# Performance work log

Hardware: AMD Instinct MI355X
Metric: run time of the kernel (lower is better)

## Reference

```python
import jax, jax.numpy as jnp
import numpy as np

IN_DIM = 1024
OUT_DIM = 1024
NUM_EXPERTS = 8
TOP_K = 2
B = 8192


def setup_inputs() -> dict:
    key = jax.random.key(0)
    ks = jax.random.split(key, 8)
    s_in = 1.0 / np.sqrt(IN_DIM)
    s_out = 1.0 / np.sqrt(OUT_DIM)
    return {
        "x": jax.random.normal(ks[0], (B, IN_DIM), dtype=jnp.float32),
        # router Linear(in_dim, num_experts)
        "rw": jax.random.uniform(ks[1], (IN_DIM, NUM_EXPERTS), jnp.float32, -s_in, s_in),
        "rb": jax.random.uniform(ks[2], (NUM_EXPERTS,), jnp.float32, -s_in, s_in),
        # expert MLPs stacked along expert axis
        "w1": jax.random.uniform(ks[3], (NUM_EXPERTS, IN_DIM, OUT_DIM), jnp.float32, -s_in, s_in),
        "b1": jax.random.uniform(ks[4], (NUM_EXPERTS, OUT_DIM), jnp.float32, -s_in, s_in),
        "w2": jax.random.uniform(ks[5], (NUM_EXPERTS, OUT_DIM, OUT_DIM), jnp.float32, -s_out, s_out),
        "b2": jax.random.uniform(ks[6], (NUM_EXPERTS, OUT_DIM), jnp.float32, -s_out, s_out),
    }


def reference(x, rw, rb, w1, b1, w2, b2):
    # ---- TopkRouter ----
    logits = x @ rw + rb                                  # [B, E]
    topk_vals, topk_idx = jax.lax.top_k(logits, TOP_K)    # [B, K]
    neg_inf = jnp.full_like(logits, -jnp.inf)
    rows = jnp.arange(logits.shape[0])[:, None]
    sparse_logits = neg_inf.at[rows, topk_idx].set(topk_vals)
    gating = jax.nn.softmax(sparse_logits, axis=-1)       # zeros outside top-k

    # ---- experts: dense compute, gating weights are exactly 0 for
    # non-selected experts so the weighted combine matches the masked
    # dispatch of the original module. ----
    h = jax.nn.relu(jnp.einsum('bi,eio->beo', x, w1) + b1[None])   # [B, E, out]
    y = jnp.einsum('beh,eho->beo', h, w2) + b2[None]               # [B, E, out]
    fused = jnp.einsum('beo,be->bo', y, gating)                    # [B, out]
    return fused, gating
```

## Files before the change

kernel.cpp:

```cpp
#include <hip/hip_runtime.h>
#include <hip/hip_bf16.h>
#include <cstdint>
#include <cstddef>

#define IN_DIM 1024
#define OUT_DIM 1024
#define NE 8
#define NTOK 8192
#define MT_TILES 20
#define RBLK 512

typedef __bf16 bf16x8 __attribute__((ext_vector_type(8)));
typedef float f32x4 __attribute__((ext_vector_type(4)));
typedef unsigned short ushort8v __attribute__((ext_vector_type(8)));

__device__ __forceinline__ unsigned short f2bf(float f) {
    unsigned u = __float_as_uint(f);
    unsigned r = 0x7fffu + ((u >> 16) & 1u);
    return (unsigned short)((u + r) >> 16);
}

__device__ __forceinline__ void bf2x(unsigned u, float& lo, float& hi) {
    lo = __uint_as_float(u << 16);
    hi = __uint_as_float(u & 0xffff0000u);
}

__device__ __forceinline__ void async16(void* lds, const void* g) {
    __builtin_amdgcn_global_load_lds(
        (const __attribute__((address_space(1))) unsigned int*)g,
        (__attribute__((address_space(3))) unsigned int*)lds,
        16, 0, 0);
}

__device__ __forceinline__ void convert_tile(
    const float* __restrict__ src, unsigned short* __restrict__ dst,
    int kt, int nt, int t, float* tile ) {
    int r = t >> 2, cq = (t & 3) * 16;
#pragma unroll
    for (int q = 0; q < 4; ++q) {
        float4 v = *(const float4*)(src + (size_t)(kt + r) * 1024 + nt + cq + q * 4);
        tile[r * 69 + cq + q * 4 + 0] = v.x;
        tile[r * 69 + cq + q * 4 + 1] = v.y;
        tile[r * 69 + cq + q * 4 + 2] = v.z;
        tile[r * 69 + cq + q * 4 + 3] = v.w;
    }
    __syncthreads();
    int n2 = t >> 3, k8 = (t & 7) * 8;
#pragma unroll
    for (int q = 0; q < 2; ++q) {
        int n = n2 + q * 32;
        ushort8v o;
#pragma unroll
        for (int i = 0; i < 8; ++i) o[i] = f2bf(tile[(k8 + i) * 69 + n]);
        *(ushort8v*)(dst + (size_t)(nt + n) * 1024 + kt + k8) = o;
    }
}

__global__ __launch_bounds__(256) void prep_kernel(
    const float* __restrict__ w1, unsigned short* __restrict__ w1T,
    const float* __restrict__ x, const float* __restrict__ rw,
    const float* __restrict__ rb,
    unsigned short* __restrict__ xb,
    float* __restrict__ gating, int* __restrict__ enc,
    float2* __restrict__ gw, int* __restrict__ cnt) {
    __shared__ float lds_f[NE * IN_DIM];
    int b = blockIdx.x;
    int t = threadIdx.x;
    if (b < RBLK) {
        float* srw = lds_f;
        if (b == 0 && t < NE) cnt[t] = 0;
#pragma unroll
        for (int i = 0; i < 4; ++i) {
            int k = t + i * 256;
            float4 a = *(const float4*)(rw + (size_t)k * NE);
            float4 bq = *(const float4*)(rw + (size_t)k * NE + 4);
            srw[0 * IN_DIM + k] = a.x;  srw[1 * IN_DIM + k] = a.y;
            srw[2 * IN_DIM + k] = a.z;  srw[3 * IN_DIM + k] = a.w;
            srw[4 * IN_DIM + k] = bq.x; srw[5 * IN_DIM + k] = bq.y;
            srw[6 * IN_DIM + k] = bq.z; srw[7 * IN_DIM + k] = bq.w;
        }
        __syncthreads();
        int wave = t >> 6, lane = t & 63;
        for (int tt = 0; tt < 4; ++tt) {
            int tok = b * 16 + wave * 4 + tt;
            const float* xrow = x + (size_t)tok * IN_DIM;
            unsigned short* xbrow = xb + (size_t)tok * IN_DIM;
            float acc[NE] = {0, 0, 0, 0, 0, 0, 0, 0};
#pragma unroll
            for (int i = 0; i < 4; ++i) {
                int k = i * 256 + lane * 4;
                float4 xv = *(const float4*)(xrow + k);
                ushort4 o;
                o.x = f2bf(xv.x); o.y = f2bf(xv.y); o.z = f2bf(xv.z); o.w = f2bf(xv.w);
                *(ushort4*)(xbrow + k) = o;
#pragma unroll
                for (int e = 0; e < NE; ++e) {
                    float4 wv = *(const float4*)(srw + e * IN_DIM + k);
                    acc[e] = fmaf(xv.x, wv.x, fmaf(xv.y, wv.y, fmaf(xv.z, wv.z, fmaf(xv.w, wv.w, acc[e]))));
                }
            }
#pragma unroll
            for (int e = 0; e < NE; ++e) {
#pragma unroll
                for (int off = 32; off > 0; off >>= 1) acc[e] += __shfl_xor(acc[e], off);
                acc[e] += rb[e];
            }
            int e0 = 0; float v0 = acc[0];
#pragma unroll
            for (int e = 1; e < NE; ++e) if (acc[e] > v0) { v0 = acc[e]; e0 = e; }
            int e1 = -1; float v1 = -3.4e38f;
#pragma unroll
            for (int e = 0; e < NE; ++e) if (e != e0 && acc[e] > v1) { v1 = acc[e]; e1 = e; }
            float tg = __expf(v1 - v0);
            float inv = 1.0f / (1.0f + tg);
            float g0 = inv, g1 = tg * inv;
            if (lane < NE) gating[(size_t)tok * NE + lane] = (lane == e0) ? g0 : ((lane == e1) ? g1 : 0.0f);
            if (lane == 0) {
                enc[tok] = e0 | (e1 << 8);
                gw[tok] = make_float2(g0, g1);
            }
        }
    } else {
        int cb = b - RBLK;
        int z = cb >> 8;
        int kt = ((cb >> 4) & 15) * 64, nt = (cb & 15) * 64;
        convert_tile(w1 + (size_t)z * IN_DIM * OUT_DIM,
                     w1T + (size_t)z * IN_DIM * OUT_DIM, kt, nt, t, lds_f);
    }
}

__global__ __launch_bounds__(256) void bucket_kernel(
    const int* __restrict__ enc,
    int* __restrict__ bidx, int* __restrict__ slots, int* __restrict__ cnt,
    const float* __restrict__ w2, unsigned short* __restrict__ w2T) {
    int b = blockIdx.x;
    int t = threadIdx.x;
    if (b < NTOK / 256) {
        int tok = b * 256 + t;
        int lane = t & 63;
        int v = enc[tok];
        int e0 = v & 0xff, e1 = (v >> 8) & 0xff;
        unsigned long long below = (1ull << lane) - 1ull;
        int p0 = 0, p1 = 0;
#pragma unroll
        for (int e = 0; e < NE; ++e) {
            unsigned long long m0 = __ballot(e0 == e);
            unsigned long long m1 = __ballot(e1 == e);
            int c0 = __popcll(m0), c1 = __popcll(m1);
            int base = 0;
            if (lane == 0 && (c0 + c1)) base = atomicAdd(&cnt[e], c0 + c1);
            base = __shfl(base, 0);
            if (e0 == e) p0 = base + __popcll(m0 & below);
            if (e1 == e) p1 = base + c0 + __popcll(m1 & below);
        }
        bidx[e0 * NTOK + p0] = tok;
        bidx[e1 * NTOK + p1] = tok;
        slots[2 * tok + 0] = (e0 << 13) | p0;
        slots[2 * tok + 1] = (e1 << 13) | p1;
    } else {
        __shared__ float tile[64 * 69];
        int cb = b - NTOK / 256;
        int z = cb >> 8;
        int kt = ((cb >> 4) & 15) * 64, nt = (cb & 15) * 64;
        convert_tile(w2 + (size_t)z * OUT_DIM * OUT_DIM,
                     w2T + (size_t)z * OUT_DIM * OUT_DIM, kt, nt, t, tile);
    }
}

__device__ __forceinline__ int prefix_cnt(const int* __restrict__ cnt, int e) {
    int s = 0;
    for (int i = 0; i < NE; ++i) s += (i < e) ? cnt[i] : 0;
    return s;
}

__device__ __forceinline__ void kstep(const unsigned short* Ab,
                                      const unsigned short* Bb,
                                      f32x4 (&acc)[4][4], int wm, int wn,
                                      int lhalf, int slot) {
    bf16x8 av[4], bv[4];
#pragma unroll
    for (int i = 0; i < 4; ++i)
        av[i] = *(const bf16x8*)(Ab + (wm * 32 + i * 8 + lhalf) * 64 + slot);
#pragma unroll
    for (int j = 0; j < 4; ++j)
        bv[j] = *(const bf16x8*)(Bb + (wn * 32 + j * 8 + lhalf) * 64 + slot);
#pragma unroll
    for (int i = 0; i < 4; ++i)
#pragma unroll
        for (int j = 0; j < 4; ++j)
            acc[i][j] = __builtin_amdgcn_mfma_f32_16x16x32_bf16(av[i], bv[j], acc[i][j], 0, 0, 0);
}


__global__ __launch_bounds__(256) void gemm1_kernel(
    const unsigned short* __restrict__ xb, const unsigned short* __restrict__ w1T,
    const float* __restrict__ b1, const int* __restrict__ bidx,
    const int* __restrict__ cnt,
    unsigned short* __restrict__ H) {
    int b = blockIdx.x;
    int e = b & 7;
    int t2 = b >> 3;
    int nt = t2 & 7;
    int mt = t2 >> 3;
    int n_e = cnt[e];
    if (mt * 128 >= n_e) return;
    __shared__ __attribute__((aligned(16))) unsigned short As[3][64 * 64];
    __shared__ __attribute__((aligned(16))) unsigned short Bs[3][64 * 64];
    int t = threadIdx.x, wave = t >> 6, lane = t & 63;
    const int* be = bidx + e * NTOK;
    const unsigned short* agp[2]; const unsigned short* bgp[2];
    int ldsoff[2];
#pragma unroll
    for (int is = 0; is < 2; ++is) {
        int c = is * 256 + t;
        int line = c >> 3;
        int chunkg = (c & 7) ^ (line & 7);
        int sub = chunkg >> 2;
        int growl = 2 * line + sub;
        int growlB = (line >> 5) * 64 + (line & 7) * 8 + sub * 4 + ((line >> 3) & 3);
        int gcol = (chunkg & 3) * 8;
        int gra = mt * 128 + growl;
        int grac = gra < n_e ? gra : n_e - 1;
        agp[is] = xb + (size_t)be[grac] * IN_DIM + gcol;
        bgp[is] = w1T + ((size_t)e * OUT_DIM + nt * 128 + growlB) * IN_DIM + gcol;
        ldsoff[is] = (is * 256 + wave * 64) * 8;
    }
    int wm = wave & 1, wn = wave >> 1;
    int quad = lane >> 4, l15 = lane & 15;
    int lhalf = l15 >> 1;
    int slot = (((l15 & 1) * 4 + quad) ^ lhalf) * 8;
    f32x4 zero4 = {0.f, 0.f, 0.f, 0.f};
    f32x4 acc[4][4];
#pragma unroll
    for (int i = 0; i < 4; ++i)
#pragma unroll
        for (int j = 0; j < 4; ++j) acc[i][j] = zero4;

#pragma unroll
    for (int pt = 0; pt < 2; ++pt)
#pragma unroll
        for (int is = 0; is < 2; ++is) {
            async16(&As[pt][ldsoff[is]], agp[is] + pt * 32);
            async16(&Bs[pt][ldsoff[is]], bgp[is] + pt * 32);
        }
    int cb = 0, sb = 2;
    for (int it = 0; it < 31; ++it) {
        asm volatile("s_waitcnt vmcnt(4)\n\ts_barrier" ::: "memory");
        if (it < 30) {
            int ktn = (it + 2) * 32;
#pragma unroll
            for (int is = 0; is < 2; ++is) {
                async16(&As[sb][ldsoff[is]], agp[is] + ktn);
                async16(&Bs[sb][ldsoff[is]], bgp[is] + ktn);
            }
        }
        kstep(As[cb], Bs[cb], acc, wm, wn, lhalf, slot);
        cb = (cb == 2) ? 0 : cb + 1;
        sb = (sb == 2) ? 0 : sb + 1;
    }
    asm volatile("s_waitcnt vmcnt(0)\n\ts_barrier" ::: "memory");
    kstep(As[cb], Bs[cb], acc, wm, wn, lhalf, slot);

    int hbase = prefix_cnt(cnt, e);
    const float* b1e = b1 + (size_t)e * OUT_DIM;
    int n0 = nt * 128 + wn * 64 + l15 * 4;
    float4 bias = *(const float4*)(b1e + n0);
#pragma unroll
    for (int i = 0; i < 4; ++i) {
        int m0 = mt * 128 + wm * 64 + i * 16 + quad * 4;
#pragma unroll
        for (int r = 0; r < 4; ++r) {
            int gm = m0 + r;
            if (gm < n_e) {
                float h0 = acc[i][0][r] + bias.x; h0 = h0 > 0.f ? h0 : 0.f;
                float h1 = acc[i][1][r] + bias.y; h1 = h1 > 0.f ? h1 : 0.f;
                float h2 = acc[i][2][r] + bias.z; h2 = h2 > 0.f ? h2 : 0.f;
                float h3 = acc[i][3][r] + bias.w; h3 = h3 > 0.f ? h3 : 0.f;
                ushort4 o;
                o.x = f2bf(h0); o.y = f2bf(h1); o.z = f2bf(h2); o.w = f2bf(h3);
                *(ushort4*)(H + (size_t)(hbase + gm) * OUT_DIM + n0) = o;
            }
        }
    }
}

__global__ __launch_bounds__(256) void gemm2_kernel(
    const unsigned short* __restrict__ H, const unsigned short* __restrict__ w2T,
    const int* __restrict__ cnt,
    unsigned short* __restrict__ Y) {
    int b = blockIdx.x;
    int e = b & 7;
    int t2 = b >> 3;
    int nt = t2 & 7;
    int mt = t2 >> 3;
    int n_e = cnt[e];
    if (mt * 128 >= n_e) return;
    __shared__ __attribute__((aligned(16))) unsigned short As[3][64 * 64];
    __shared__ __attribute__((aligned(16))) unsigned short Bs[3][64 * 64];
    int t = threadIdx.x, wave = t >> 6, lane = t & 63;
    int hbase = prefix_cnt(cnt, e);
    const unsigned short* agp[2]; const unsigned short* bgp[2];
    int ldsoff[2];
#pragma unroll
    for (int is = 0; is < 2; ++is) {
        int c = is * 256 + t;
        int line = c >> 3;
        int chunkg = (c & 7) ^ (line & 7);
        int sub = chunkg >> 2;
        int growl = 2 * line + sub;
        int growlB = (line >> 5) * 64 + (line & 7) * 8 + sub * 4 + ((line >> 3) & 3);
        int gcol = (chunkg & 3) * 8;
        int gra = mt * 128 + growl;
        int grac = gra < n_e ? gra : n_e - 1;
        agp[is] = H + (size_t)(hbase + grac) * OUT_DIM + gcol;
        bgp[is] = w2T + ((size_t)e * OUT_DIM + nt * 128 + growlB) * OUT_DIM + gcol;
        ldsoff[is] = (is * 256 + wave * 64) * 8;
    }
    int wm = wave & 1, wn = wave >> 1;
    int quad = lane >> 4, l15 = lane & 15;
    int lhalf = l15 >> 1;
    int slot = (((l15 & 1) * 4 + quad) ^ lhalf) * 8;
    f32x4 zero4 = {0.f, 0.f, 0.f, 0.f};
    f32x4 acc[4][4];
#pragma unroll
    for (int i = 0; i < 4; ++i)
#pragma unroll
        for (int j = 0; j < 4; ++j) acc[i][j] = zero4;

#pragma unroll
    for (int pt = 0; pt < 2; ++pt)
#pragma unroll
        for (int is = 0; is < 2; ++is) {
            async16(&As[pt][ldsoff[is]], agp[is] + pt * 32);
            async16(&Bs[pt][ldsoff[is]], bgp[is] + pt * 32);
        }
    int cb = 0, sb = 2;
    for (int it = 0; it < 31; ++it) {
        asm volatile("s_waitcnt vmcnt(4)\n\ts_barrier" ::: "memory");
        if (it < 30) {
            int ktn = (it + 2) * 32;
#pragma unroll
            for (int is = 0; is < 2; ++is) {
                async16(&As[sb][ldsoff[is]], agp[is] + ktn);
                async16(&Bs[sb][ldsoff[is]], bgp[is] + ktn);
            }
        }
        kstep(As[cb], Bs[cb], acc, wm, wn, lhalf, slot);
        cb = (cb == 2) ? 0 : cb + 1;
        sb = (sb == 2) ? 0 : sb + 1;
    }
    asm volatile("s_waitcnt vmcnt(0)\n\ts_barrier" ::: "memory");
    kstep(As[cb], Bs[cb], acc, wm, wn, lhalf, slot);

    int n0 = nt * 128 + wn * 64 + l15 * 4;
#pragma unroll
    for (int i = 0; i < 4; ++i) {
        int m0 = mt * 128 + wm * 64 + i * 16 + quad * 4;
#pragma unroll
        for (int r = 0; r < 4; ++r) {
            int gm = m0 + r;
            if (gm < n_e) {
                ushort4 o;
                o.x = f2bf(acc[i][0][r]); o.y = f2bf(acc[i][1][r]);
                o.z = f2bf(acc[i][2][r]); o.w = f2bf(acc[i][3][r]);
                *(ushort4*)(Y + (size_t)(hbase + gm) * OUT_DIM + n0) = o;
            }
        }
    }
}

__global__ __launch_bounds__(256) void combine_kernel(
    const unsigned short* __restrict__ Y, const float* __restrict__ b2,
    const float2* __restrict__ gw, const int* __restrict__ slots,
    const int* __restrict__ cnt, float* __restrict__ out) {
    int t = threadIdx.x, wave = t >> 6, lane = t & 63;
    int tok = blockIdx.x * 4 + wave;
    int pre[NE];
    {
        int s = 0;
#pragma unroll
        for (int i = 0; i < NE; ++i) { pre[i] = s; s += cnt[i]; }
    }
    int s0 = slots[2 * tok], s1 = slots[2 * tok + 1];
    int e0 = s0 >> 13, e1 = s1 >> 13;
    int r0 = pre[e0] + (s0 & 8191);
    int r1 = pre[e1] + (s1 & 8191);
    float2 g = gw[tok];
    const unsigned short* y0 = Y + (size_t)r0 * OUT_DIM;
    const unsigned short* y1 = Y + (size_t)r1 * OUT_DIM;
    const float* c0 = b2 + (size_t)e0 * OUT_DIM;
    const float* c1 = b2 + (size_t)e1 * OUT_DIM;
    float* orow = out + (size_t)tok * OUT_DIM;
#pragma unroll
    for (int i = 0; i < 2; ++i) {
        int c = i * 512 + lane * 8;
        uint4 ua = *(const uint4*)(y0 + c);
        uint4 ub = *(const uint4*)(y1 + c);
        float a[8], b[8];
        bf2x(ua.x, a[0], a[1]); bf2x(ua.y, a[2], a[3]);
        bf2x(ua.z, a[4], a[5]); bf2x(ua.w, a[6], a[7]);
        bf2x(ub.x, b[0], b[1]); bf2x(ub.y, b[2], b[3]);
        bf2x(ub.z, b[4], b[5]); bf2x(ub.w, b[6], b[7]);
        float4 p0 = *(const float4*)(c0 + c);
        float4 p1 = *(const float4*)(c0 + c + 4);
        float4 q0 = *(const float4*)(c1 + c);
        float4 q1 = *(const float4*)(c1 + c + 4);
        float o[8];
        o[0] = g.x * (a[0] + p0.x) + g.y * (b[0] + q0.x);
        o[1] = g.x * (a[1] + p0.y) + g.y * (b[1] + q0.y);
        o[2] = g.x * (a[2] + p0.z) + g.y * (b[2] + q0.z);
        o[3] = g.x * (a[3] + p0.w) + g.y * (b[3] + q0.w);
        o[4] = g.x * (a[4] + p1.x) + g.y * (b[4] + q1.x);
        o[5] = g.x * (a[5] + p1.y) + g.y * (b[5] + q1.y);
        o[6] = g.x * (a[6] + p1.z) + g.y * (b[6] + q1.z);
        o[7] = g.x * (a[7] + p1.w) + g.y * (b[7] + q1.w);
        *(float4*)(orow + c) = make_float4(o[0], o[1], o[2], o[3]);
        *(float4*)(orow + c + 4) = make_float4(o[4], o[5], o[6], o[7]);
    }
}

extern "C" void kernel_launch(void* const* d_in, const int* in_sizes, int n_in,
                              void* d_out, int out_size, void* d_ws, size_t ws_size,
                              hipStream_t stream) {
    const float* x  = (const float*)d_in[0];
    const float* rw = (const float*)d_in[1];
    const float* rb = (const float*)d_in[2];
    const float* w1 = (const float*)d_in[3];
    const float* b1 = (const float*)d_in[4];
    const float* w2 = (const float*)d_in[5];
    const float* b2 = (const float*)d_in[6];
    float* out = (float*)d_out;
    float* gating = out + (size_t)NTOK * OUT_DIM;

    char* ws = (char*)d_ws;
    unsigned short* xb  = (unsigned short*)(ws + 0);
    unsigned short* Y   = (unsigned short*)(ws + 0);
    unsigned short* w1T = (unsigned short*)(ws + 16777216);
    unsigned short* w2T = (unsigned short*)(ws + 33554432);
    unsigned short* H   = (unsigned short*)(ws + 50331648);
    int*   bidx  = (int*)(ws + 83886080);
    int*   slots = (int*)(ws + 84148224);
    int*   cnt   = (int*)(ws + 84213760);
    int*    enc  = (int*)(ws + 84213888);
    float2* gw   = (float2*)(ws + 84246656);

    prep_kernel<<<RBLK + 8 * 16 * 16, 256, 0, stream>>>(
        w1, w1T, x, rw, rb, xb, gating, enc, gw, cnt);
    bucket_kernel<<<NTOK / 256 + 8 * 16 * 16, 256, 0, stream>>>(
        enc, bidx, slots, cnt, w2, w2T);
    gemm1_kernel<<<8 * 8 * MT_TILES, 256, 0, stream>>>(xb, w1T, b1, bidx, cnt, H);
    gemm2_kernel<<<8 * 8 * MT_TILES, 256, 0, stream>>>(H, w2T, cnt, Y);
    combine_kernel<<<NTOK / 4, 256, 0, stream>>>(Y, b2, gw, slots, cnt, out);
    (void)in_sizes; (void)n_in; (void)out_size; (void)ws_size;
}
```

Before: 279.0 us.

## Fuse token bucketing and w2 conversion into the router prep kernel

The separate bucket kernel is removed. Each router block now assigns its 16 tokens to expert buckets with a wave-level ballot and atomics right after routing, and the w2 transpose/convert tiles run as extra blocks of the same prep launch. The counter reset moves to a memset before the launch. This saves a kernel launch and the enc round-trip through global memory, at the cost of more atomics (one set per 16 tokens instead of per 64) and a different bucket ordering.

```diff
diff --git a/kernel.cpp b/kernel.cpp
--- a/kernel.cpp
+++ b/kernel.cpp
@@ -57,18 +57,20 @@
 }
 
 __global__ __launch_bounds__(256) void prep_kernel(
-    const float* __restrict__ w1, unsigned short* __restrict__ w1T,
+    const float* __restrict__ w1, const float* __restrict__ w2,
+    unsigned short* __restrict__ w1T, unsigned short* __restrict__ w2T,
     const float* __restrict__ x, const float* __restrict__ rw,
     const float* __restrict__ rb,
     unsigned short* __restrict__ xb,
-    float* __restrict__ gating, int* __restrict__ enc,
-    float2* __restrict__ gw, int* __restrict__ cnt) {
+    float* __restrict__ gating,
+    float2* __restrict__ gw, int* __restrict__ cnt,
+    int* __restrict__ bidx, int* __restrict__ slots) {
     __shared__ float lds_f[NE * IN_DIM];
+    __shared__ int ebuf[32];
     int b = blockIdx.x;
     int t = threadIdx.x;
     if (b < RBLK) {
         float* srw = lds_f;
-        if (b == 0 && t < NE) cnt[t] = 0;
 #pragma unroll
         for (int i = 0; i < 4; ++i) {
             int k = t + i * 256;
@@ -82,7 +84,8 @@
         __syncthreads();
         int wave = t >> 6, lane = t & 63;
         for (int tt = 0; tt < 4; ++tt) {
-            int tok = b * 16 + wave * 4 + tt;
+            int idx = wave * 4 + tt;
+            int tok = b * 16 + idx;
             const float* xrow = x + (size_t)tok * IN_DIM;
             unsigned short* xbrow = xb + (size_t)tok * IN_DIM;
             float acc[NE] = {0, 0, 0, 0, 0, 0, 0, 0};
@@ -116,54 +119,45 @@
             float g0 = inv, g1 = tg * inv;
             if (lane < NE) gating[(size_t)tok * NE + lane] = (lane == e0) ? g0 : ((lane == e1) ? g1 : 0.0f);
             if (lane == 0) {
-                enc[tok] = e0 | (e1 << 8);
+                ebuf[2 * idx + 0] = e0;
+                ebuf[2 * idx + 1] = e1;
                 gw[tok] = make_float2(g0, g1);
             }
         }
-    } else {
+        __syncthreads();
+        if (t < 64) {
+            bool active = t < 32;
+            int myE = active ? ebuf[t] : 0xff;
+            unsigned long long below = (1ull << t) - 1ull;
+            int pos = 0;
+#pragma unroll
+            for (int e = 0; e < NE; ++e) {
+                unsigned long long m = __ballot(active && myE == e);
+                int c = __popcll(m);
+                int base = 0;
+                if (t == 0 && c) base = atomicAdd(&cnt[e], c);
+                base = __shfl(base, 0);
+                if (active && myE == e) pos = base + __popcll(m & below);
+            }
+            if (active) {
+                int tok = b * 16 + (t >> 1);
+                int which = t & 1;
+                bidx[myE * NTOK + pos] = tok;
+                slots[2 * tok + which] = (myE << 13) | pos;
+            }
+        }
+    } else if (b < RBLK + 2048) {
         int cb = b - RBLK;
         int z = cb >> 8;
         int kt = ((cb >> 4) & 15) * 64, nt = (cb & 15) * 64;
         convert_tile(w1 + (size_t)z * IN_DIM * OUT_DIM,
                      w1T + (size_t)z * IN_DIM * OUT_DIM, kt, nt, t, lds_f);
-    }
-}
-
-__global__ __launch_bounds__(256) void bucket_kernel(
-    const int* __restrict__ enc,
-    int* __restrict__ bidx, int* __restrict__ slots, int* __restrict__ cnt,
-    const float* __restrict__ w2, unsigned short* __restrict__ w2T) {
-    int b = blockIdx.x;
-    int t = threadIdx.x;
-    if (b < NTOK / 256) {
-        int tok = b * 256 + t;
-        int lane = t & 63;
-        int v = enc[tok];
-        int e0 = v & 0xff, e1 = (v >> 8) & 0xff;
-        unsigned long long below = (1ull << lane) - 1ull;
-        int p0 = 0, p1 = 0;
-#pragma unroll
-        for (int e = 0; e < NE; ++e) {
-            unsigned long long m0 = __ballot(e0 == e);
-            unsigned long long m1 = __ballot(e1 == e);
-            int c0 = __popcll(m0), c1 = __popcll(m1);
-            int base = 0;
-            if (lane == 0 && (c0 + c1)) base = atomicAdd(&cnt[e], c0 + c1);
-            base = __shfl(base, 0);
-            if (e0 == e) p0 = base + __popcll(m0 & below);
-            if (e1 == e) p1 = base + c0 + __popcll(m1 & below);
-        }
-        bidx[e0 * NTOK + p0] = tok;
-        bidx[e1 * NTOK + p1] = tok;
-        slots[2 * tok + 0] = (e0 << 13) | p0;
-        slots[2 * tok + 1] = (e1 << 13) | p1;
     } else {
-        __shared__ float tile[64 * 69];
-        int cb = b - NTOK / 256;
+        int cb = b - RBLK - 2048;
         int z = cb >> 8;
         int kt = ((cb >> 4) & 15) * 64, nt = (cb & 15) * 64;
         convert_tile(w2 + (size_t)z * OUT_DIM * OUT_DIM,
-                     w2T + (size_t)z * OUT_DIM * OUT_DIM, kt, nt, t, tile);
+                     w2T + (size_t)z * OUT_DIM * OUT_DIM, kt, nt, t, lds_f);
     }
 }
 
@@ -441,13 +435,11 @@
     int*   bidx  = (int*)(ws + 83886080);
     int*   slots = (int*)(ws + 84148224);
     int*   cnt   = (int*)(ws + 84213760);
-    int*    enc  = (int*)(ws + 84213888);
     float2* gw   = (float2*)(ws + 84246656);
 
-    prep_kernel<<<RBLK + 8 * 16 * 16, 256, 0, stream>>>(
-        w1, w1T, x, rw, rb, xb, gating, enc, gw, cnt);
-    bucket_kernel<<<NTOK / 256 + 8 * 16 * 16, 256, 0, stream>>>(
-        enc, bidx, slots, cnt, w2, w2T);
+    hipMemsetAsync(cnt, 0, NE * sizeof(int), stream);
+    prep_kernel<<<RBLK + 4096, 256, 0, stream>>>(
+        w1, w2, w1T, w2T, x, rw, rb, xb, gating, gw, cnt, bidx, slots);
     gemm1_kernel<<<8 * 8 * MT_TILES, 256, 0, stream>>>(xb, w1T, b1, bidx, cnt, H);
     gemm2_kernel<<<8 * 8 * MT_TILES, 256, 0, stream>>>(H, w2T, cnt, Y);
     combine_kernel<<<NTOK / 4, 256, 0, stream>>>(Y, b2, gw, slots, cnt, out);
```

After: 311.7 us. 11.7% more time.
